# Performance work log

Measured on AMD Instinct MI355X. Metric: run time of the kernel, lower is better.

The kernel has to match this reference:

```python
import jax, jax.numpy as jnp
import numpy as np

EPS = float(np.finfo(np.float32).eps)
B, MZ, NF = 8192, 2000, 2048
W_INT, W_PROB, W_WS, W_MORGAN = 0.1, 0.3, 0.5, 0.1
POS_W = 5.0


def _bce_logits(x, y):
    # numerically-stable BCEWithLogits, elementwise
    return jnp.maximum(x, 0.0) - x * y + jnp.log1p(jnp.exp(-jnp.abs(x)))


def setup_inputs() -> dict:
    key = jax.random.key(0)
    k = jax.random.split(key, 6)
    return {
        "pred_intensities": jax.random.normal(k[0], (B, MZ), jnp.float32),
        "pred_probs_logits": jax.random.normal(k[1], (B, MZ), jnp.float32),
        "pred_morgan_logits": jax.random.normal(k[2], (B, NF), jnp.float32),
        "true_intensities": jax.random.uniform(k[3], (B, MZ), dtype=jnp.float32),
        "true_probs": jax.random.uniform(k[4], (B, MZ), dtype=jnp.float32),
        "true_morgan": jax.random.randint(k[5], (B, NF), 0, 2).astype(jnp.int32),
    }


def reference(pred_intensities, pred_probs_logits, pred_morgan_logits,
              true_intensities, true_probs, true_morgan):
    # --- prob loss: BCEWithLogits with positive-class upweighting ---
    bce = _bce_logits(pred_probs_logits, true_probs)
    w = jnp.where(true_probs > 0.5, POS_W, 1.0)
    prob_loss = jnp.mean(bce * w)

    # --- intensity loss: MSE masked to true peaks ---
    iw = (true_probs > 0.5).astype(jnp.float32)
    intensity_loss = jnp.sum(iw * (pred_intensities - true_intensities) ** 2) / (jnp.sum(iw) + EPS)

    # --- Wasserstein-1 loss (original detaches pred -> no grad; exact EMD on 1D
    #     grid with cost |i-j|/(MZ-1+EPS) == scaled L1 distance of CDFs) ---
    pred_prob = jax.nn.sigmoid(pred_probs_logits)
    pred_dist = jax.nn.relu(pred_intensities) * pred_prob
    pred_dist = pred_dist / (pred_dist.sum(axis=1, keepdims=True) + EPS)
    true_un = true_intensities * true_probs
    true_dist = true_un / (true_un.sum(axis=1, keepdims=True) + EPS)
    # per-sample renormalization as in the python loop
    p = pred_dist / (pred_dist.sum(axis=1, keepdims=True) + EPS)
    q = true_dist / (true_dist.sum(axis=1, keepdims=True) + EPS)
    scale = 1.0 / (float(MZ - 1) + EPS)  # cost matrix M = |i-j| / (max + EPS)
    cdf_diff = jnp.cumsum(p - q, axis=1)          # [B, MZ]
    w1 = jnp.sum(jnp.abs(cdf_diff[:, :-1]), axis=1) * scale  # exact 1D EMD
    psum = p.sum(axis=1)
    qsum = q.sum(axis=1)
    valid = (qsum > EPS).astype(jnp.float32)       # counted iff true mass > EPS
    per_sample = jnp.where(psum > EPS, w1, 1.0)    # pred degenerate -> penalty 1.0
    nvalid = jnp.sum(valid)
    ws_loss = jnp.where(nvalid > 0,
                        jnp.sum(per_sample * valid) / jnp.maximum(nvalid, 1.0),
                        0.0)
    ws_loss = jax.lax.stop_gradient(ws_loss)  # original converts to python float

    # --- morgan fingerprint loss: mean BCEWithLogits ---
    morgan_loss = jnp.mean(_bce_logits(pred_morgan_logits, true_morgan.astype(jnp.float32)))

    total = (W_PROB * prob_loss + W_INT * intensity_loss
             + W_WS * ws_loss + W_MORGAN * morgan_loss)
    total = jnp.where(jnp.isnan(total) | jnp.isinf(total), 100000.0, total)
    return total
```

## Files before the change

kernel.cpp:

```cpp
#include <hip/hip_runtime.h>
#include <cmath>

#define EPSF 1.1920928955078125e-07f

constexpr int BB = 8192;
constexpr int MZ = 2000;
constexpr int NF = 2048;
constexpr int MORGAN_BLOCKS = 2048;
constexpr float W_INT = 0.1f, W_PROB = 0.3f, W_WS = 0.5f, W_MORGAN = 0.1f;
constexpr float POS_W = 5.0f;

constexpr int PB_STRIDE = BB;
constexpr int PBM_OFF = 5 * BB;

__device__ inline float waveReduce(float v) {
#pragma unroll
  for (int off = 32; off > 0; off >>= 1) v += __shfl_down(v, off, 64);
  return v;
}

__device__ inline double waveReduceD(double v) {
#pragma unroll
  for (int off = 32; off > 0; off >>= 1) v += __shfl_down(v, off, 64);
  return v;
}

__device__ inline float bceLogits(float x, float y) {
  return fmaxf(x, 0.f) - x * y + log1pf(expf(-fabsf(x)));
}

__global__ __launch_bounds__(256) void row_kernel(
    const float* __restrict__ pi, const float* __restrict__ pl,
    const float* __restrict__ ti, const float* __restrict__ tp,
    float* __restrict__ pb) {
  __shared__ float red[4][8];
  __shared__ float bc[2];
  __shared__ float wtot[4];

  const int tid = threadIdx.x;
  const int lane = tid & 63;
  const int wid = tid >> 6;
  const int bid = blockIdx.x;
  const long base = (long)bid * MZ;
  const int i0 = tid * 8;

  float a[8], b[8];
  float s_bce = 0.f, s_sq = 0.f, s_iw = 0.f, la = 0.f, lb = 0.f;

  if (i0 + 8 <= MZ) {
    const float4* ppi = (const float4*)(pi + base + i0);
    const float4* ppl = (const float4*)(pl + base + i0);
    const float4* pti = (const float4*)(ti + base + i0);
    const float4* ptp = (const float4*)(tp + base + i0);
    float4 vpi0 = ppi[0], vpi1 = ppi[1];
    float4 vpl0 = ppl[0], vpl1 = ppl[1];
    float4 vti0 = pti[0], vti1 = pti[1];
    float4 vtp0 = ptp[0], vtp1 = ptp[1];
    float xpi[8] = {vpi0.x, vpi0.y, vpi0.z, vpi0.w, vpi1.x, vpi1.y, vpi1.z, vpi1.w};
    float xpl[8] = {vpl0.x, vpl0.y, vpl0.z, vpl0.w, vpl1.x, vpl1.y, vpl1.z, vpl1.w};
    float xti[8] = {vti0.x, vti0.y, vti0.z, vti0.w, vti1.x, vti1.y, vti1.z, vti1.w};
    float xtp[8] = {vtp0.x, vtp0.y, vtp0.z, vtp0.w, vtp1.x, vtp1.y, vtp1.z, vtp1.w};
#pragma unroll
    for (int j = 0; j < 8; ++j) {
      const float x = xpl[j];
      const float y = xtp[j];
      const float em = expf(-fabsf(x));
      const float bce = fmaxf(x, 0.f) - x * y + log1pf(em);
      const bool pos = (y > 0.5f);
      s_bce += bce * (pos ? POS_W : 1.f);
      const float d = xpi[j] - xti[j];
      if (pos) { s_sq = fmaf(d, d, s_sq); s_iw += 1.f; }
      const float sig = (x >= 0.f) ? (1.f / (1.f + em)) : (em / (1.f + em));
      const float av = fmaxf(xpi[j], 0.f) * sig;
      const float bv = xti[j] * y;
      a[j] = av; b[j] = bv;
      la += av; lb += bv;
    }
  } else {
#pragma unroll
    for (int j = 0; j < 8; ++j) { a[j] = 0.f; b[j] = 0.f; }
  }

  float v0 = waveReduce(la);
  float v1 = waveReduce(lb);
  float v2 = waveReduce(s_bce);
  float v3 = waveReduce(s_sq);
  float v4 = waveReduce(s_iw);
  if (lane == 0) {
    red[wid][0] = v0; red[wid][1] = v1; red[wid][2] = v2;
    red[wid][3] = v3; red[wid][4] = v4;
  }
  __syncthreads();
  if (tid == 0) {
    const float s1  = red[0][0] + red[1][0] + red[2][0] + red[3][0];
    const float st1 = red[0][1] + red[1][1] + red[2][1] + red[3][1];
    bc[0] = s1; bc[1] = st1;
    pb[0 * PB_STRIDE + bid] = red[0][2] + red[1][2] + red[2][2] + red[3][2];
    pb[1 * PB_STRIDE + bid] = red[0][3] + red[1][3] + red[2][3] + red[3][3];
    pb[2 * PB_STRIDE + bid] = red[0][4] + red[1][4] + red[2][4] + red[3][4];
  }
  __syncthreads();
  const float s1 = bc[0], st1 = bc[1];

  const float s2 = s1 / (s1 + EPSF);
  const float scaleP = 1.f / ((s1 + EPSF) * (s2 + EPSF));
  const float st2 = st1 / (st1 + EPSF);
  const float scaleQ = 1.f / ((st1 + EPSF) * (st2 + EPSF));

  float run = 0.f;
#pragma unroll
  for (int j = 0; j < 8; ++j) {
    run += a[j] * scaleP - b[j] * scaleQ;
    a[j] = run;
  }

  float sc = run;
#pragma unroll
  for (int off = 1; off < 64; off <<= 1) {
    const float t = __shfl_up(sc, off, 64);
    if (lane >= off) sc += t;
  }
  if (lane == 63) wtot[wid] = sc;
  __syncthreads();
  float woff = 0.f;
#pragma unroll
  for (int w = 0; w < 4; ++w) woff += (w < wid) ? wtot[w] : 0.f;
  const float excl = sc - run + woff;

  float labs = 0.f;
#pragma unroll
  for (int j = 0; j < 8; ++j) {
    if (i0 + j < MZ - 1) labs += fabsf(excl + a[j]);
  }
  labs = waveReduce(labs);
  if (lane == 0) red[wid][0] = labs;
  __syncthreads();
  if (tid == 0) {
    const float t = red[0][0] + red[1][0] + red[2][0] + red[3][0];
    const float w1 = t * (1.f / (1999.0f + EPSF));
    const float psum = s2 / (s2 + EPSF);
    const float qsum = st2 / (st2 + EPSF);
    const float valid = (qsum > EPSF) ? 1.f : 0.f;
    const float per = (psum > EPSF) ? w1 : 1.f;
    pb[3 * PB_STRIDE + bid] = per * valid;
    pb[4 * PB_STRIDE + bid] = valid;
  }
}

__global__ __launch_bounds__(256) void morgan_kernel(
    const float* __restrict__ x, const int* __restrict__ y,
    float* __restrict__ pbm) {
  __shared__ float red[4];
  const long n4 = (long)BB * NF / 4;
  const long stride = (long)gridDim.x * blockDim.x;
  float ls = 0.f;
  for (long i = (long)blockIdx.x * blockDim.x + threadIdx.x; i < n4; i += stride) {
    const float4 xv = ((const float4*)x)[i];
    const int4 yv = ((const int4*)y)[i];
    ls += bceLogits(xv.x, (float)yv.x);
    ls += bceLogits(xv.y, (float)yv.y);
    ls += bceLogits(xv.z, (float)yv.z);
    ls += bceLogits(xv.w, (float)yv.w);
  }
  ls = waveReduce(ls);
  const int lane = threadIdx.x & 63, wid = threadIdx.x >> 6;
  if (lane == 0) red[wid] = ls;
  __syncthreads();
  if (threadIdx.x == 0)
    pbm[blockIdx.x] = red[0] + red[1] + red[2] + red[3];
}

__global__ __launch_bounds__(1024) void reduce_finalize_kernel(
    const float* __restrict__ ws, float* __restrict__ out) {
  __shared__ double red[16][8];
  const int tid = threadIdx.x;
  const int lane = tid & 63, wid = tid >> 6;

  double acc[6] = {0, 0, 0, 0, 0, 0};
#pragma unroll
  for (int k = 0; k < 5; ++k)
    for (int i = tid; i < BB; i += 1024)
      acc[k] += (double)ws[k * PB_STRIDE + i];
  for (int i = tid; i < MORGAN_BLOCKS; i += 1024)
    acc[5] += (double)ws[PBM_OFF + i];

#pragma unroll
  for (int k = 0; k < 6; ++k) acc[k] = waveReduceD(acc[k]);
  if (lane == 0) {
#pragma unroll
    for (int k = 0; k < 6; ++k) red[wid][k] = acc[k];
  }
  __syncthreads();
  if (tid == 0) {
    double t[6];
#pragma unroll
    for (int k = 0; k < 6; ++k) {
      double s = 0.0;
      for (int w = 0; w < 16; ++w) s += red[w][k];
      t[k] = s;
    }
    const double prob = t[0] / ((double)BB * (double)MZ);
    const double inten = t[1] / (t[2] + (double)EPSF);
    const double nv = t[4];
    const double ws_loss = (nv > 0.0) ? (t[3] / fmax(nv, 1.0)) : 0.0;
    const double morgan = t[5] / ((double)BB * (double)NF);
    double tot = (double)W_PROB * prob + (double)W_INT * inten +
                 (double)W_WS * ws_loss + (double)W_MORGAN * morgan;
    float r = (float)tot;
    if (isnan(r) || isinf(r)) r = 100000.0f;
    out[0] = r;
  }
}

extern "C" void kernel_launch(void* const* d_in, const int* in_sizes, int n_in,
                              void* d_out, int out_size, void* d_ws, size_t ws_size,
                              hipStream_t stream) {
  const float* pred_int = (const float*)d_in[0];
  const float* pred_pl  = (const float*)d_in[1];
  const float* pred_mg  = (const float*)d_in[2];
  const float* true_int = (const float*)d_in[3];
  const float* true_pr  = (const float*)d_in[4];
  const int*   true_mg  = (const int*)d_in[5];
  float* ws = (float*)d_ws;

  row_kernel<<<BB, 256, 0, stream>>>(pred_int, pred_pl, true_int, true_pr, ws);
  morgan_kernel<<<MORGAN_BLOCKS, 256, 0, stream>>>(pred_mg, true_mg, ws + PBM_OFF);
  reduce_finalize_kernel<<<1, 1024, 0, stream>>>(ws, (float*)d_out);
}
```

Before: 388.3 us.

## Fuse row and morgan kernels into one interleaved launch with fast math

Merges the per-row loss kernel and the morgan BCE kernel into a single launch, interleaving one morgan block after every four row blocks so both workloads share the GPU and the launch boundary disappears. It also swaps expf/log1pf for the __expf/__logf intrinsics, uses a hardware reciprocal for the sigmoid, and vectorizes the final reduction's loads as float4. The fast intrinsics trade a little accuracy, and __logf(1+em) loses precision when em is small. The kernel is memory-bound at roughly 400MB, so the gains are likely modest.

```diff
diff --git a/kernel.cpp b/kernel.cpp
--- a/kernel.cpp
+++ b/kernel.cpp
@@ -7,6 +7,7 @@
 constexpr int MZ = 2000;
 constexpr int NF = 2048;
 constexpr int MORGAN_BLOCKS = 2048;
+constexpr int FUSED_BLOCKS = BB + MORGAN_BLOCKS;
 constexpr float W_INT = 0.1f, W_PROB = 0.3f, W_WS = 0.5f, W_MORGAN = 0.1f;
 constexpr float POS_W = 5.0f;
 
@@ -25,14 +26,16 @@
   return v;
 }
 
-__device__ inline float bceLogits(float x, float y) {
-  return fmaxf(x, 0.f) - x * y + log1pf(expf(-fabsf(x)));
-}
-
-__global__ __launch_bounds__(256) void row_kernel(
-    const float* __restrict__ pi, const float* __restrict__ pl,
-    const float* __restrict__ ti, const float* __restrict__ tp,
-    float* __restrict__ pb) {
+__device__ inline float bceFast(float x, float y) {
+  const float em = __expf(-fabsf(x));
+  return fmaxf(x, 0.f) - x * y + __logf(1.f + em);
+}
+
+__device__ inline void row_body(int bid, const float* __restrict__ pi,
+                                const float* __restrict__ pl,
+                                const float* __restrict__ ti,
+                                const float* __restrict__ tp,
+                                float* __restrict__ pb) {
   __shared__ float red[4][8];
   __shared__ float bc[2];
   __shared__ float wtot[4];
@@ -40,7 +43,6 @@
   const int tid = threadIdx.x;
   const int lane = tid & 63;
   const int wid = tid >> 6;
-  const int bid = blockIdx.x;
   const long base = (long)bid * MZ;
   const int i0 = tid * 8;
 
@@ -64,13 +66,14 @@
     for (int j = 0; j < 8; ++j) {
       const float x = xpl[j];
       const float y = xtp[j];
-      const float em = expf(-fabsf(x));
-      const float bce = fmaxf(x, 0.f) - x * y + log1pf(em);
+      const float em = __expf(-fabsf(x));
+      const float bce = fmaxf(x, 0.f) - x * y + __logf(1.f + em);
       const bool pos = (y > 0.5f);
       s_bce += bce * (pos ? POS_W : 1.f);
       const float d = xpi[j] - xti[j];
       if (pos) { s_sq = fmaf(d, d, s_sq); s_iw += 1.f; }
-      const float sig = (x >= 0.f) ? (1.f / (1.f + em)) : (em / (1.f + em));
+      const float inv = __builtin_amdgcn_rcpf(1.f + em);
+      const float sig = (x >= 0.f) ? inv : em * inv;
       const float av = fmaxf(xpi[j], 0.f) * sig;
       const float bv = xti[j] * y;
       a[j] = av; b[j] = bv;
@@ -147,27 +150,41 @@
   }
 }
 
-__global__ __launch_bounds__(256) void morgan_kernel(
-    const float* __restrict__ x, const int* __restrict__ y,
-    float* __restrict__ pbm) {
-  __shared__ float red[4];
+__device__ inline void morgan_body(int mbid, const float* __restrict__ x,
+                                   const int* __restrict__ y,
+                                   float* __restrict__ pbm) {
+  __shared__ float mred[4];
   const long n4 = (long)BB * NF / 4;
-  const long stride = (long)gridDim.x * blockDim.x;
+  const long stride = (long)MORGAN_BLOCKS * 256;
   float ls = 0.f;
-  for (long i = (long)blockIdx.x * blockDim.x + threadIdx.x; i < n4; i += stride) {
+  for (long i = (long)mbid * 256 + threadIdx.x; i < n4; i += stride) {
     const float4 xv = ((const float4*)x)[i];
     const int4 yv = ((const int4*)y)[i];
-    ls += bceLogits(xv.x, (float)yv.x);
-    ls += bceLogits(xv.y, (float)yv.y);
-    ls += bceLogits(xv.z, (float)yv.z);
-    ls += bceLogits(xv.w, (float)yv.w);
+    ls += bceFast(xv.x, (float)yv.x);
+    ls += bceFast(xv.y, (float)yv.y);
+    ls += bceFast(xv.z, (float)yv.z);
+    ls += bceFast(xv.w, (float)yv.w);
   }
   ls = waveReduce(ls);
   const int lane = threadIdx.x & 63, wid = threadIdx.x >> 6;
-  if (lane == 0) red[wid] = ls;
+  if (lane == 0) mred[wid] = ls;
   __syncthreads();
   if (threadIdx.x == 0)
-    pbm[blockIdx.x] = red[0] + red[1] + red[2] + red[3];
+    pbm[mbid] = mred[0] + mred[1] + mred[2] + mred[3];
+}
+
+__global__ __launch_bounds__(256) void fused_kernel(
+    const float* __restrict__ pi, const float* __restrict__ pl,
+    const float* __restrict__ ti, const float* __restrict__ tp,
+    const float* __restrict__ mx, const int* __restrict__ my,
+    float* __restrict__ ws) {
+  const int q = blockIdx.x / 5;
+  const int r = blockIdx.x % 5;
+  if (r < 4) {
+    row_body(q * 4 + r, pi, pl, ti, tp, ws);
+  } else {
+    morgan_body(q, mx, my, ws + PBM_OFF);
+  }
 }
 
 __global__ __launch_bounds__(1024) void reduce_finalize_kernel(
@@ -178,11 +195,20 @@
 
   double acc[6] = {0, 0, 0, 0, 0, 0};
 #pragma unroll
-  for (int k = 0; k < 5; ++k)
-    for (int i = tid; i < BB; i += 1024)
-      acc[k] += (double)ws[k * PB_STRIDE + i];
-  for (int i = tid; i < MORGAN_BLOCKS; i += 1024)
-    acc[5] += (double)ws[PBM_OFF + i];
+  for (int k = 0; k < 5; ++k) {
+    const float4* v = (const float4*)(ws + k * PB_STRIDE);
+    for (int i = tid; i < BB / 4; i += 1024) {
+      const float4 f = v[i];
+      acc[k] += (double)f.x + (double)f.y + (double)f.z + (double)f.w;
+    }
+  }
+  {
+    const float4* v = (const float4*)(ws + PBM_OFF);
+    for (int i = tid; i < MORGAN_BLOCKS / 4; i += 1024) {
+      const float4 f = v[i];
+      acc[5] += (double)f.x + (double)f.y + (double)f.z + (double)f.w;
+    }
+  }
 
 #pragma unroll
   for (int k = 0; k < 6; ++k) acc[k] = waveReduceD(acc[k]);
@@ -223,7 +249,7 @@
   const int*   true_mg  = (const int*)d_in[5];
   float* ws = (float*)d_ws;
 
-  row_kernel<<<BB, 256, 0, stream>>>(pred_int, pred_pl, true_int, true_pr, ws);
-  morgan_kernel<<<MORGAN_BLOCKS, 256, 0, stream>>>(pred_mg, true_mg, ws + PBM_OFF);
+  fused_kernel<<<FUSED_BLOCKS, 256, 0, stream>>>(
+      pred_int, pred_pl, true_int, true_pr, pred_mg, true_mg, ws);
   reduce_finalize_kernel<<<1, 1024, 0, stream>>>(ws, (float*)d_out);
 }
```

After: 348.6 us. 10.2% less time.
